# Kernel tuning notes

Hardware: AMD Instinct MI355X
Metric: run time of the kernel (lower is better)

Reference implementation:

```python
import jax, jax.numpy as jnp
import numpy as np

# Grid constants from init_kwargs: output_shape = [1, 10, 200, 176, 64]
D, H, W, C = 10, 200, 176, 64
N_VOX = 30000


def _conv_block(x, w, scale, bias, stride, pad):
    # x: [N,C,D,H,W]; w: [O,I,kd,kh,kw]; ZeroPad3d then valid Conv3d,
    # then fused (inference) BatchNorm3d + ReLU.
    x = jnp.pad(x, ((0, 0), (0, 0), (pad[0], pad[0]), (pad[1], pad[1]), (pad[2], pad[2])))
    x = jax.lax.conv_general_dilated(
        x, w, window_strides=stride, padding='VALID',
        dimension_numbers=('NCDHW', 'OIDHW', 'NCDHW'))
    s = scale[None, :, None, None, None]
    b = bias[None, :, None, None, None]
    return jax.nn.relu(x * s + b)


def setup_inputs() -> dict:
    key = jax.random.key(0)
    kf, kd, kh, kw, k1, k2, k3, ks = jax.random.split(key, 8)
    voxel_features = jax.random.normal(kf, (N_VOX, C), dtype=jnp.float32)
    # coors columns: (batch_idx, d, h, w) each in range
    b_idx = jnp.zeros((N_VOX,), dtype=jnp.int32)  # batch_size = 1
    d_idx = jax.random.randint(kd, (N_VOX,), 0, D, dtype=jnp.int32)
    h_idx = jax.random.randint(kh, (N_VOX,), 0, H, dtype=jnp.int32)
    w_idx = jax.random.randint(kw, (N_VOX,), 0, W, dtype=jnp.int32)
    coors = jnp.stack([b_idx, d_idx, h_idx, w_idx], axis=1)
    fan = 1.0 / np.sqrt(C * 27)
    W1 = jax.random.normal(k1, (64, C, 3, 3, 3), dtype=jnp.float32) * fan
    W2 = jax.random.normal(k2, (64, 64, 3, 3, 3), dtype=jnp.float32) * fan
    W3 = jax.random.normal(k3, (64, 64, 3, 3, 3), dtype=jnp.float32) * fan
    ks1, ks2, ks3 = jax.random.split(ks, 3)
    scale1 = jax.random.uniform(ks1, (64,), dtype=jnp.float32, minval=0.5, maxval=1.5)
    scale2 = jax.random.uniform(ks2, (64,), dtype=jnp.float32, minval=0.5, maxval=1.5)
    scale3 = jax.random.uniform(ks3, (64,), dtype=jnp.float32, minval=0.5, maxval=1.5)
    bias1 = jax.random.normal(jax.random.fold_in(ks1, 1), (64,), dtype=jnp.float32) * 0.1
    bias2 = jax.random.normal(jax.random.fold_in(ks2, 1), (64,), dtype=jnp.float32) * 0.1
    bias3 = jax.random.normal(jax.random.fold_in(ks3, 1), (64,), dtype=jnp.float32) * 0.1
    return {
        'voxel_features': voxel_features, 'coors': coors, 'batch_size': 1,
        'W1': W1, 'scale1': scale1, 'bias1': bias1,
        'W2': W2, 'scale2': scale2, 'bias2': bias2,
        'W3': W3, 'scale3': scale3, 'bias3': bias3,
    }


def reference(voxel_features, coors, batch_size,
              W1, scale1, bias1, W2, scale2, bias2, W3, scale3, bias3):
    # scatter_nd: sparse voxel features -> dense [B, D, H, W, C]
    dense = jnp.zeros((batch_size, D, H, W, C), dtype=voxel_features.dtype)
    dense = dense.at[coors[:, 0], coors[:, 1], coors[:, 2], coors[:, 3]].set(voxel_features)
    x = dense.transpose(0, 4, 1, 2, 3)  # [B, C, D, H, W]
    # middle_conv: Pad(1)+Conv3d s=(2,1,1); Pad(0,1,1)+Conv3d s=1; Pad(1)+Conv3d s=(2,1,1)
    x = _conv_block(x, W1, scale1, bias1, (2, 1, 1), (1, 1, 1))   # D: 10 -> 5
    x = _conv_block(x, W2, scale2, bias2, (1, 1, 1), (0, 1, 1))   # D: 5 -> 3
    x = _conv_block(x, W3, scale3, bias3, (2, 1, 1), (1, 1, 1))   # D: 3 -> 2
    N, Cc, Dd, Hh, Ww = x.shape
    return x.reshape(N, Cc * Dd, Hh, Ww)  # [B, 128, H, W]
```

## Files before the change

### kernel.cpp

```cpp
#include <hip/hip_runtime.h>
#include <cstddef>

#define HH 200
#define WW 176
#define HP 202
#define WP 178
#define D_IN 10
#define D1 5
#define D2 3
#define D3 2
#define SLICE ((size_t)HP * WP * 64)

#define LA_BYTES 38912

typedef _Float16 h8 __attribute__((ext_vector_type(8)));
typedef float f4 __attribute__((ext_vector_type(4)));

__device__ __forceinline__ void gl_lds16(const void* g, void* l) {
    __builtin_amdgcn_global_load_lds(
        (const __attribute__((address_space(1))) void*)g,
        (__attribute__((address_space(3))) void*)l, 16, 0, 0);
}

__global__ __launch_bounds__(256) void prep_k(const float* __restrict__ W1,
                                              const float* __restrict__ W2,
                                              const float* __restrict__ W3,
                                              _Float16* __restrict__ wdst,
                                              _Float16* __restrict__ A2,
                                              _Float16* __restrict__ A3,
                                              const int* __restrict__ coors,
                                              int* __restrict__ winner, int nvox) {
    const int b = blockIdx.x;
    if (b < 8) {
        _Float16* base = (b < D1) ? (A2 + (size_t)b * SLICE) : (A3 + (size_t)(b - D1) * SLICE);
        const h8 z = {};
        for (int t = threadIdx.x; t < 6080; t += 256) {
            size_t off;
            if (t < 2848) {
                int r = t / 1424, c = t - r * 1424;
                off = (size_t)(r ? (HP - 1) : 0) * WP * 64 + (size_t)c * 8;
            } else {
                int u = t - 2848;
                int c = u / 1616, v = u - c * 1616;
                int hr = v >> 3, o = v & 7;
                off = ((size_t)hr * WP + (c ? (WP - 1) : 0)) * 64 + (size_t)o * 8;
            }
            *(h8*)(base + off) = z;
        }
    } else if (b < 8 + 1296) {
        int idx = (b - 8) * 256 + threadIdx.x;
        if (idx < 3 * 27 * 64 * 64) {
            int set = idx / 110592;
            int r = idx - set * 110592;
            const float* src = set == 0 ? W1 : (set == 1 ? W2 : W3);
            int ci = r & 63;
            int co = (r >> 6) & 63;
            int tap = r >> 12;
            wdst[set * 110592 + tap * 4096 + (ci >> 3) * 512 + co * 8 + (ci & 7)] =
                (_Float16)src[(co * 64 + ci) * 27 + tap];
        }
    } else {
        int v = (b - 1304) * 256 + threadIdx.x;
        if (v < nvox) {
            int d = coors[v * 4 + 1], h = coors[v * 4 + 2], w = coors[v * 4 + 3];
            atomicMax(&winner[(d * HH + h) * WW + w], v + 1);
        }
    }
}

__global__ __launch_bounds__(256) void scatter_k(const float* __restrict__ feat,
                                                 const int* __restrict__ coors,
                                                 const int* __restrict__ winner,
                                                 _Float16* __restrict__ A, int nvox) {
    int v = blockIdx.x * 4 + (threadIdx.x >> 6);
    int ci = threadIdx.x & 63;
    if (v >= nvox) return;
    int d = coors[v * 4 + 1], h = coors[v * 4 + 2], w = coors[v * 4 + 3];
    if (winner[(d * HH + h) * WW + w] != v + 1) return;
    int P = w + 1;
    int swz = (((ci >> 3) ^ (P & 7)) << 3) | (ci & 7);
    A[(size_t)d * SLICE + ((size_t)(h + 1) * WP + P) * 64 + swz] = (_Float16)feat[v * 64 + ci];
}

template <int FINAL>
__global__ __launch_bounds__(256, 4) void conv_mfma_k(
    const _Float16* __restrict__ in, void* __restrict__ outp,
    const _Float16* __restrict__ wt,
    const float* __restrict__ scale, const float* __restrict__ bias,
    int inD, int strideD, int padD) {
    __shared__ char smem_raw[LA_BYTES];
    _Float16* la = (_Float16*)smem_raw;

    const int lane = threadIdx.x & 63;
    const int wave = threadIdx.x >> 6;
    const int l16 = lane & 15;
    const int quad = lane >> 4;
    const int h0 = blockIdx.y * 4;
    const int wb = blockIdx.x * 48;
    const int d = blockIdx.z;

    int kd_lo = padD - d * strideD; if (kd_lo < 0) kd_lo = 0;
    int kd_hi = inD - 1 - d * strideD + padD; if (kd_hi > 2) kd_hi = 2;

    f4 acc[3][4];
#pragma unroll
    for (int mt = 0; mt < 3; ++mt)
#pragma unroll
        for (int nt = 0; nt < 4; ++nt) acc[mt][nt] = (f4){0.f, 0.f, 0.f, 0.f};

    for (int kd = kd_lo; kd <= kd_hi; ++kd) {
        const int zd = d * strideD + kd - padD;
        const _Float16* __restrict__ aplane = in + (size_t)zd * SLICE;
        const _Float16* __restrict__ wkd = wt + (size_t)kd * 9 * 4096;

        __syncthreads();
        for (int j = wave; j < 38; j += 4) {
            int c = j * 64 + lane;
            if (c > 2399) c = 2399;
            int r = c / 400;
            int rem = c - r * 400;
            int px = rem >> 3, s = rem & 7;
            int g = wb + px; if (g > 177) g = 177;
            gl_lds16(aplane + ((size_t)(h0 + r) * WP + g) * 64 + s * 8,
                     smem_raw + j * 1024);
        }
        h8 bc[4], bn[4];
#pragma unroll
        for (int nt = 0; nt < 4; ++nt)
            bc[nt] = *(const h8*)(wkd + (quad << 9) + ((nt * 16 + l16) << 3));
        __syncthreads();

#pragma unroll
        for (int p = 0; p < 18; ++p) {
            const int t = p >> 1;
            const int ch = p & 1;
            const int kh = t / 3;
            const int kw = t - 3 * kh;
            const int q = ch * 4 + quad;

            const int pn = (p < 17) ? p + 1 : 17;
            const int tn = pn >> 1, chn = pn & 1;
#pragma unroll
            for (int nt = 0; nt < 4; ++nt)
                bn[nt] = *(const h8*)(wkd + tn * 4096 + ((chn * 4 + quad) << 9) +
                                      ((nt * 16 + l16) << 3));

#pragma unroll
            for (int mt = 0; mt < 3; ++mt) {
                const int px = mt * 16 + l16 + kw;
                h8 a = *(const h8*)(la + ((size_t)(wave + kh) * 50 + px) * 64 +
                                    ((q ^ (px & 7)) << 3));
#pragma unroll
                for (int nt = 0; nt < 4; ++nt)
                    acc[mt][nt] = __builtin_amdgcn_mfma_f32_16x16x32_f16(
                        a, bc[nt], acc[mt][nt], 0, 0, 0);
            }

#pragma unroll
            for (int nt = 0; nt < 4; ++nt) bc[nt] = bn[nt];
        }
    }

    const int h = h0 + wave;
    if (FINAL) {
#pragma unroll
        for (int nt = 0; nt < 4; ++nt) {
            const int co = nt * 16 + l16;
            const float s = scale[co];
            const float bb = bias[co];
#pragma unroll
            for (int mt = 0; mt < 3; ++mt) {
                const int w0 = wb + mt * 16 + quad * 4;
                if (w0 < WW) {
                    f4 v;
#pragma unroll
                    for (int r = 0; r < 4; ++r) {
                        float x = acc[mt][nt][r] * s + bb;
                        v[r] = x > 0.f ? x : 0.f;
                    }
                    *(f4*)((float*)outp + (((size_t)(co * 2 + d)) * HH + h) * WW + w0) = v;
                }
            }
        }
    } else {
        __syncthreads();
        _Float16* ep = (_Float16*)smem_raw + (size_t)wave * (48 * 72);
#pragma unroll
        for (int nt = 0; nt < 4; ++nt) {
            const int co = nt * 16 + l16;
            const float s = scale[co];
            const float bb = bias[co];
#pragma unroll
            for (int mt = 0; mt < 3; ++mt) {
#pragma unroll
                for (int r = 0; r < 4; ++r) {
                    float x = acc[mt][nt][r] * s + bb;
                    x = x > 0.f ? x : 0.f;
                    ep[(mt * 16 + quad * 4 + r) * 72 + co] = (_Float16)x;
                }
            }
        }
        const int lim = (WW - wb) * 8;
#pragma unroll
        for (int cv = 0; cv < 6; ++cv) {
            if (cv * 64 < lim) {
                const int c2 = cv * 64 + lane;
                const int pxl = c2 >> 3, s = c2 & 7;
                h8 v = *(const h8*)(ep + pxl * 72 + s * 8);
                const int P = wb + pxl + 1;
                *(h8*)((_Float16*)outp + (size_t)d * SLICE +
                       ((size_t)(h + 1) * WP + P) * 64 + ((s ^ (P & 7)) << 3)) = v;
            }
        }
    }
}

extern "C" void kernel_launch(void* const* d_in, const int* in_sizes, int n_in,
                              void* d_out, int out_size, void* d_ws, size_t ws_size,
                              hipStream_t stream) {
    const float* feat   = (const float*)d_in[0];
    const int*   coors  = (const int*)d_in[1];
    const float* W1     = (const float*)d_in[3];
    const float* scale1 = (const float*)d_in[4];
    const float* bias1  = (const float*)d_in[5];
    const float* W2     = (const float*)d_in[6];
    const float* scale2 = (const float*)d_in[7];
    const float* bias2  = (const float*)d_in[8];
    const float* W3     = (const float*)d_in[9];
    const float* scale3 = (const float*)d_in[10];
    const float* bias3  = (const float*)d_in[11];
    const int nvox = in_sizes[0] / 64;

    const size_t nA1 = (size_t)D_IN * SLICE;
    const size_t nWin = (size_t)D_IN * HH * WW;
    const size_t nA2 = (size_t)D1 * SLICE;
    const size_t nA3 = (size_t)D2 * SLICE;
    const size_t nWT = (size_t)27 * 64 * 64;

    _Float16* A1 = (_Float16*)d_ws;
    int* win = (int*)(A1 + nA1);
    _Float16* A2 = (_Float16*)(win + nWin);
    _Float16* A3 = A2 + nA2;
    _Float16* wt1 = A3 + nA3;
    _Float16* wt2 = wt1 + nWT;
    _Float16* wt3 = wt2 + nWT;

    hipMemsetAsync(d_ws, 0, nA1 * sizeof(_Float16) + nWin * sizeof(int), stream);

    const int win_blk = (nvox + 255) / 256;
    prep_k<<<8 + 1296 + win_blk, 256, 0, stream>>>(W1, W2, W3, wt1, A2, A3,
                                                   coors, win, nvox);
    scatter_k<<<(nvox + 3) / 4, 256, 0, stream>>>(feat, coors, win, A1, nvox);

    dim3 blk(256);
    conv_mfma_k<0><<<dim3(4, 50, D1), blk, 0, stream>>>(A1, A2, wt1, scale1, bias1, D_IN, 2, 1);
    conv_mfma_k<0><<<dim3(4, 50, D2), blk, 0, stream>>>(A2, A3, wt2, scale2, bias2, D1, 1, 0);
    conv_mfma_k<1><<<dim3(4, 50, D3), blk, 0, stream>>>(A3, (float*)d_out, wt3, scale3, bias3, D2, 2, 1);
}
```

Measured before the change: 191.3 us.

## Stage conv weights in double-buffered LDS and double rows per block

Each conv block now covers 8 output rows with 8 waves instead of 4. Per-tap weight slices are staged into LDS with async global-to-LDS loads into two alternating buffers, and the weight layout is swizzled to avoid LDS bank conflicts. This replaces per-lane register prefetch of weights straight from global memory. It adds two barriers per tap and raises LDS use to about 80KB, which lowers the number of resident blocks and halves the grid size.

```diff
diff --git a/kernel.cpp b/kernel.cpp
--- a/kernel.cpp
+++ b/kernel.cpp
@@ -11,7 +11,9 @@
 #define D3 2
 #define SLICE ((size_t)HP * WP * 64)
 
-#define LA_BYTES 38912
+#define LA_BYTES 64512
+#define LB_BYTES 8192
+#define LDS_TOTAL (LA_BYTES + 2 * LB_BYTES)
 
 typedef _Float16 h8 __attribute__((ext_vector_type(8)));
 typedef float f4 __attribute__((ext_vector_type(4)));
@@ -56,7 +58,8 @@
             int ci = r & 63;
             int co = (r >> 6) & 63;
             int tap = r >> 12;
-            wdst[set * 110592 + tap * 4096 + (ci >> 3) * 512 + co * 8 + (ci & 7)] =
+            int s = ci >> 3, j = ci & 7;
+            wdst[set * 110592 + tap * 4096 + co * 64 + (((s ^ (co & 7)) << 3) | j)] =
                 (_Float16)src[(co * 64 + ci) * 27 + tap];
         }
     } else {
@@ -83,19 +86,21 @@
 }
 
 template <int FINAL>
-__global__ __launch_bounds__(256, 4) void conv_mfma_k(
+__global__ __launch_bounds__(512, 4) void conv_mfma_k(
     const _Float16* __restrict__ in, void* __restrict__ outp,
     const _Float16* __restrict__ wt,
     const float* __restrict__ scale, const float* __restrict__ bias,
     int inD, int strideD, int padD) {
-    __shared__ char smem_raw[LA_BYTES];
+    __shared__ char smem_raw[LDS_TOTAL];
     _Float16* la = (_Float16*)smem_raw;
+    char* lb0 = smem_raw + LA_BYTES;
+    char* lb1 = smem_raw + LA_BYTES + LB_BYTES;
 
     const int lane = threadIdx.x & 63;
     const int wave = threadIdx.x >> 6;
     const int l16 = lane & 15;
     const int quad = lane >> 4;
-    const int h0 = blockIdx.y * 4;
+    const int h0 = blockIdx.y * 8;
     const int wb = blockIdx.x * 48;
     const int d = blockIdx.z;
 
@@ -113,10 +118,9 @@
         const _Float16* __restrict__ aplane = in + (size_t)zd * SLICE;
         const _Float16* __restrict__ wkd = wt + (size_t)kd * 9 * 4096;
 
-        __syncthreads();
-        for (int j = wave; j < 38; j += 4) {
+        for (int j = wave; j < 63; j += 8) {
             int c = j * 64 + lane;
-            if (c > 2399) c = 2399;
+            if (c > 3999) c = 3999;
             int r = c / 400;
             int rem = c - r * 400;
             int px = rem >> 3, s = rem & 7;
@@ -124,40 +128,50 @@
             gl_lds16(aplane + ((size_t)(h0 + r) * WP + g) * 64 + s * 8,
                      smem_raw + j * 1024);
         }
-        h8 bc[4], bn[4];
-#pragma unroll
-        for (int nt = 0; nt < 4; ++nt)
-            bc[nt] = *(const h8*)(wkd + (quad << 9) + ((nt * 16 + l16) << 3));
-        __syncthreads();
-
-#pragma unroll
-        for (int p = 0; p < 18; ++p) {
-            const int t = p >> 1;
-            const int ch = p & 1;
+        gl_lds16(wkd + (size_t)(wave * 64 + lane) * 8, lb0 + wave * 1024);
+
+#pragma unroll
+        for (int t = 0; t < 9; ++t) {
             const int kh = t / 3;
             const int kw = t - 3 * kh;
-            const int q = ch * 4 + quad;
-
-            const int pn = (p < 17) ? p + 1 : 17;
-            const int tn = pn >> 1, chn = pn & 1;
-#pragma unroll
-            for (int nt = 0; nt < 4; ++nt)
-                bn[nt] = *(const h8*)(wkd + tn * 4096 + ((chn * 4 + quad) << 9) +
-                                      ((nt * 16 + l16) << 3));
-
-#pragma unroll
-            for (int mt = 0; mt < 3; ++mt) {
-                const int px = mt * 16 + l16 + kw;
-                h8 a = *(const h8*)(la + ((size_t)(wave + kh) * 50 + px) * 64 +
-                                    ((q ^ (px & 7)) << 3));
+            char* lbc = (t & 1) ? lb1 : lb0;
+
+            if (t < 8) {
+                char* lbn = (t & 1) ? lb0 : lb1;
+                gl_lds16(wkd + (size_t)(t + 1) * 4096 + (size_t)(wave * 64 + lane) * 8,
+                         lbn + wave * 1024);
+                asm volatile("s_waitcnt vmcnt(1)" ::: "memory");
+            } else {
+                asm volatile("s_waitcnt vmcnt(0)" ::: "memory");
+            }
+            __builtin_amdgcn_sched_barrier(0);
+            __builtin_amdgcn_s_barrier();
+            __builtin_amdgcn_sched_barrier(0);
+
+            const _Float16* lb = (const _Float16*)lbc;
+#pragma unroll
+            for (int ch = 0; ch < 2; ++ch) {
+                const int q = ch * 4 + quad;
+                h8 b[4];
 #pragma unroll
                 for (int nt = 0; nt < 4; ++nt)
-                    acc[mt][nt] = __builtin_amdgcn_mfma_f32_16x16x32_f16(
-                        a, bc[nt], acc[mt][nt], 0, 0, 0);
-            }
-
-#pragma unroll
-            for (int nt = 0; nt < 4; ++nt) bc[nt] = bn[nt];
+                    b[nt] = *(const h8*)(lb + (nt * 16 + l16) * 64 +
+                                         ((q ^ (l16 & 7)) << 3));
+#pragma unroll
+                for (int mt = 0; mt < 3; ++mt) {
+                    const int px = mt * 16 + l16 + kw;
+                    h8 a = *(const h8*)(la + ((size_t)(wave + kh) * 50 + px) * 64 +
+                                        ((q ^ (px & 7)) << 3));
+#pragma unroll
+                    for (int nt = 0; nt < 4; ++nt)
+                        acc[mt][nt] = __builtin_amdgcn_mfma_f32_16x16x32_f16(
+                            a, b[nt], acc[mt][nt], 0, 0, 0);
+                }
+            }
+            asm volatile("s_waitcnt lgkmcnt(0)" ::: "memory");
+            __builtin_amdgcn_sched_barrier(0);
+            __builtin_amdgcn_s_barrier();
+            __builtin_amdgcn_sched_barrier(0);
         }
     }
 
@@ -183,7 +197,6 @@
             }
         }
     } else {
-        __syncthreads();
         _Float16* ep = (_Float16*)smem_raw + (size_t)wave * (48 * 72);
 #pragma unroll
         for (int nt = 0; nt < 4; ++nt) {
@@ -252,8 +265,8 @@
                                                    coors, win, nvox);
     scatter_k<<<(nvox + 3) / 4, 256, 0, stream>>>(feat, coors, win, A1, nvox);
 
-    dim3 blk(256);
-    conv_mfma_k<0><<<dim3(4, 50, D1), blk, 0, stream>>>(A1, A2, wt1, scale1, bias1, D_IN, 2, 1);
-    conv_mfma_k<0><<<dim3(4, 50, D2), blk, 0, stream>>>(A2, A3, wt2, scale2, bias2, D1, 1, 0);
-    conv_mfma_k<1><<<dim3(4, 50, D3), blk, 0, stream>>>(A3, (float*)d_out, wt3, scale3, bias3, D2, 2, 1);
-}
+    dim3 blk(512);
+    conv_mfma_k<0><<<dim3(4, 25, D1), blk, 0, stream>>>(A1, A2, wt1, scale1, bias1, D_IN, 2, 1);
+    conv_mfma_k<0><<<dim3(4, 25, D2), blk, 0, stream>>>(A2, A3, wt2, scale2, bias2, D1, 1, 0);
+    conv_mfma_k<1><<<dim3(4, 25, D3), blk, 0, stream>>>(A3, (float*)d_out, wt3, scale3, bias3, D2, 2, 1);
+}
```

New measurement: 201.9 us. +5.5%, slower.
